# Performance work log

Hardware: AMD Instinct MI355X
Metric: run time of the kernel (lower is better)

Reference implementation:

```python
import jax, jax.numpy as jnp
import numpy as np

B, T, D = 4, 2048, 512
E, H, K = 8, 512, 2


def setup_inputs() -> dict:
    key = jax.random.key(0)
    ks = jax.random.split(key, 8)
    s_in = 1.0 / np.sqrt(D)
    s_h = 1.0 / np.sqrt(H)
    return {
        "x": jax.random.normal(ks[0], (B, T, D), dtype=jnp.float32),
        "Wg": jax.random.uniform(ks[1], (D, E), jnp.float32, -s_in, s_in),
        "bg": jax.random.uniform(ks[2], (E,), jnp.float32, -s_in, s_in),
        "W1": jax.random.uniform(ks[3], (E, D, H), jnp.float32, -s_in, s_in),
        "b1": jax.random.uniform(ks[4], (E, H), jnp.float32, -s_in, s_in),
        "W2": jax.random.uniform(ks[5], (E, H, H), jnp.float32, -s_h, s_h),
        "b2": jax.random.uniform(ks[6], (E, H), jnp.float32, -s_h, s_h),
    }


def reference(x, Wg, bg, W1, b1, W2, b2):
    Bx, Tx, Dx = x.shape
    xf = x.reshape(-1, Dx)                                   # [N, D]
    # --- gate (noise_std = 0) ---
    logits = xf @ Wg + bg                                    # [N, E]
    topk_scores, topk_idx = jax.lax.top_k(logits, K)         # [N, K]
    topk_w = jax.nn.softmax(topk_scores, axis=-1)            # K=2 -> softmax over selected
    # --- experts: dense compute, then gather the selected ones ---
    h = jax.nn.gelu(jnp.einsum('nd,edh->neh', xf, W1) + b1, approximate=False)  # [N, E, H]
    y = jnp.einsum('neh,ehf->nef', h, W2) + b2               # [N, E, H]
    sel = jnp.take_along_axis(y, topk_idx[:, :, None], axis=1)  # [N, K, H]
    out = jnp.sum(topk_w[:, :, None] * sel, axis=1)          # weighted combine [N, H]
    return out.reshape(Bx, Tx, -1)
```

## Files before the change

### kernel.cpp

```cpp
#include <hip/hip_runtime.h>
#include <hip/hip_bf16.h>


typedef __bf16 bf16x8 __attribute__((ext_vector_type(8)));
typedef float  f32x4  __attribute__((ext_vector_type(4)));

#define N_TOK 8192
#define D_IN  512
#define N_EXP 8
#define H_DIM 512
#define TILE  64

static __device__ __forceinline__ unsigned short f2bf(float f) {
    union { float f; unsigned u; } v; v.f = f;
    unsigned r = v.u + 0x7FFFu + ((v.u >> 16) & 1u);
    return (unsigned short)(r >> 16);
}
static __device__ __forceinline__ float bf2f(unsigned short h) {
    union { unsigned u; float f; } v; v.u = ((unsigned)h) << 16; return v.f;
}

__global__ void __launch_bounds__(256) k_pack(const float* __restrict__ W1,
                                              const float* __restrict__ W2,
                                              unsigned short* __restrict__ w1f,
                                              unsigned short* __restrict__ w2f) {
    __shared__ float t[32][65];
    int z = blockIdx.z;
    int e = z & 7;
    const float* in = (z < 8) ? W1 : W2;
    unsigned short* out = (z < 8) ? w1f : w2f;
    int cb0 = blockIdx.x * 4;
    int kc  = blockIdx.y;
    const float* src = in + ((size_t)e * 512 + kc * 32) * 512 + blockIdx.x * 64;
    int tid = threadIdx.x;
    int r = tid >> 3, cq = (tid & 7) * 8;
    float4 v0 = *(const float4*)(src + (size_t)r * 512 + cq);
    float4 v1 = *(const float4*)(src + (size_t)r * 512 + cq + 4);
    t[r][cq + 0] = v0.x; t[r][cq + 1] = v0.y; t[r][cq + 2] = v0.z; t[r][cq + 3] = v0.w;
    t[r][cq + 4] = v1.x; t[r][cq + 5] = v1.y; t[r][cq + 6] = v1.z; t[r][cq + 7] = v1.w;
    __syncthreads();
    int g = tid >> 6, lane = tid & 63;
    int l15 = lane & 15, l4 = lane >> 4;
    unsigned v[4];
    #pragma unroll
    for (int j = 0; j < 4; ++j) {
        unsigned lo = f2bf(t[l4 * 8 + 2 * j    ][g * 16 + l15]);
        unsigned hi = f2bf(t[l4 * 8 + 2 * j + 1][g * 16 + l15]);
        v[j] = lo | (hi << 16);
    }
    size_t dst = (((size_t)(e * 32 + cb0 + g) * 16 + kc) * 512) + lane * 8;
    *(uint4*)(out + dst) = make_uint4(v[0], v[1], v[2], v[3]);
}

__global__ void __launch_bounds__(256) k_gate(const float* __restrict__ x,
                                              const float* __restrict__ Wg,
                                              const float* __restrict__ bg,
                                              unsigned char* __restrict__ sel,
                                              float2* __restrict__ w2) {
    __shared__ float part[32][8][8];
    __shared__ float lg[32][8];
    int tid = threadIdx.x;
    int t = tid >> 3, c = tid & 7;
    int n = blockIdx.x * 32 + t;
    const float4* xr = (const float4*)(x + (size_t)n * D_IN + c * 64);
    float acc[8];
    #pragma unroll
    for (int e = 0; e < 8; ++e) acc[e] = 0.f;
    #pragma unroll
    for (int j4 = 0; j4 < 16; ++j4) {
        float4 v = xr[j4];
        int k = c * 64 + j4 * 4;
        float xv[4] = {v.x, v.y, v.z, v.w};
        #pragma unroll
        for (int u = 0; u < 4; ++u) {
            float4 wlo = *(const float4*)(Wg + (size_t)(k + u) * 8);
            float4 whi = *(const float4*)(Wg + (size_t)(k + u) * 8 + 4);
            acc[0] += xv[u] * wlo.x; acc[1] += xv[u] * wlo.y;
            acc[2] += xv[u] * wlo.z; acc[3] += xv[u] * wlo.w;
            acc[4] += xv[u] * whi.x; acc[5] += xv[u] * whi.y;
            acc[6] += xv[u] * whi.z; acc[7] += xv[u] * whi.w;
        }
    }
    #pragma unroll
    for (int e = 0; e < 8; ++e) part[t][c][e] = acc[e];
    __syncthreads();
    {
        float f = bg[c];
        #pragma unroll
        for (int cc = 0; cc < 8; ++cc) f += part[t][cc][c];
        lg[t][c] = f;
    }
    __syncthreads();
    if (c == 0) {
        float best = lg[t][0]; int i1 = 0;
        #pragma unroll
        for (int j = 1; j < 8; ++j) { float v = lg[t][j]; if (v > best) { best = v; i1 = j; } }
        float best2 = -1e30f; int i2 = 0;
        #pragma unroll
        for (int j = 0; j < 8; ++j) {
            if (j == i1) continue;
            float v = lg[t][j]; if (v > best2) { best2 = v; i2 = j; }
        }
        float tt = expf(best2 - best);
        float w0 = 1.0f / (1.0f + tt);
        sel[n] = (unsigned char)(i1 | (i2 << 4));
        w2[n] = make_float2(w0, 1.0f - w0);
    }
}

__global__ void __launch_bounds__(1024) k_build(const unsigned char* __restrict__ sel,
                                                const float2* __restrict__ w2,
                                                int* __restrict__ counts,
                                                int* __restrict__ lists,
                                                float* __restrict__ wgts) {
    int e = blockIdx.x;
    __shared__ int wave_tot[16], wave_base[16];
    int tid = threadIdx.x;
    int lane = tid & 63, wv = tid >> 6;
    int base = 0;
    for (int c0 = 0; c0 < N_TOK; c0 += 1024) {
        int n = c0 + tid;
        unsigned char s = sel[n];
        bool f1 = ((s & 15) == e);
        bool f = f1 || ((s >> 4) == e);
        unsigned long long mask = __ballot(f);
        int prefix = __popcll(mask & ((1ull << lane) - 1ull));
        if (lane == 0) wave_tot[wv] = __popcll(mask);
        __syncthreads();
        if (tid < 16) {
            int wb = 0;
            for (int i = 0; i < tid; ++i) wb += wave_tot[i];
            wave_base[tid] = wb;
        }
        __syncthreads();
        if (f) {
            int pos = base + wave_base[wv] + prefix;
            lists[e * N_TOK + pos] = (n << 1) | (f1 ? 0 : 1);
            float2 w = w2[n];
            wgts[e * N_TOK + pos] = f1 ? w.x : w.y;
        }
        base += wave_base[15] + wave_tot[15];
        __syncthreads();
    }
    if (tid == 0) counts[e] = base;
}

template <bool SLOT>
__global__ void __launch_bounds__(512, 2)
k_experts(const float* __restrict__ x,
          const unsigned short* __restrict__ w1f, const float* __restrict__ b1,
          const unsigned short* __restrict__ w2f, const float* __restrict__ b2,
          const int* __restrict__ counts, const int* __restrict__ lists,
          const float* __restrict__ wgts,
          unsigned short* __restrict__ ybuf, float* __restrict__ out) {
    __shared__ unsigned short ldsA[32 * D_IN];
    __shared__ unsigned short ldsB[32 * D_IN];
    __shared__ int   tl[TILE];
    __shared__ float wl[TILE];

    int b = blockIdx.x;
    int e = b & 7;
    int tile = b >> 3;
    int cnt = counts[e];
    int row0 = tile * TILE;
    if (row0 >= cnt) return;
    int rv = min(TILE, cnt - row0);

    int tid = threadIdx.x;
    int lane = tid & 63;
    int wid = tid >> 6;
    int cw = wid * 64;
    int l15 = lane & 15, l4 = lane >> 4;

    if (tid < TILE) {
        int v = 0; float w = 0.f;
        if (tid < rv) {
            v = lists[e * N_TOK + row0 + tid];
            w = wgts [e * N_TOK + row0 + tid];
        }
        tl[tid] = v; wl[tid] = w;
    }
    __syncthreads();

    #pragma unroll
    for (int it = 0; it < 16; ++it) {
        int idx = tid + it * 512;
        int r = idx >> 7, c4 = idx & 127;
        float4 v = make_float4(0.f, 0.f, 0.f, 0.f);
        if (r < rv)
            v = ((const float4*)(x + (size_t)(tl[r] >> 1) * D_IN))[c4];
        unsigned lo = (unsigned)f2bf(v.x) | ((unsigned)f2bf(v.y) << 16);
        unsigned hi = (unsigned)f2bf(v.z) | ((unsigned)f2bf(v.w) << 16);
        int rr = r & 31;
        int off = (rr * 1024 + c4 * 8) ^ ((rr & 7) << 4);
        char* base = (r < 32) ? (char*)ldsA : (char*)ldsB;
        *(uint2*)(base + off) = make_uint2(lo, hi);
    }
    __syncthreads();

    f32x4 accA[2][4], accB[2][4];

    {
        const unsigned short* wbase = w1f + ((size_t)(e * 32 + wid * 4) * 16) * 512 + (size_t)lane * 8;
        #pragma unroll
        for (int n = 0; n < 4; ++n) {
            float bv = b1[e * H_DIM + cw + n * 16 + l15];
            #pragma unroll
            for (int m = 0; m < 2; ++m) { accA[m][n] = f32x4{bv, bv, bv, bv}; accB[m][n] = f32x4{bv, bv, bv, bv}; }
        }
        bf16x8 bb[4][4];
        #pragma unroll
        for (int n = 0; n < 4; ++n) {
            bb[0][n] = *(const bf16x8*)(wbase + (n * 16 + 0) * 512);
            bb[1][n] = *(const bf16x8*)(wbase + (n * 16 + 1) * 512);
            bb[2][n] = *(const bf16x8*)(wbase + (n * 16 + 2) * 512);
        }
        #pragma unroll
        for (int kc = 0; kc < 16; ++kc) {
            if (kc + 3 < 16) {
                #pragma unroll
                for (int n = 0; n < 4; ++n)
                    bb[(kc + 3) & 3][n] = *(const bf16x8*)(wbase + (n * 16 + kc + 3) * 512);
            }
            int k0 = kc * 32 + l4 * 8;
            bf16x8 aA[2], aB[2];
            #pragma unroll
            for (int m = 0; m < 2; ++m) {
                int row = m * 16 + l15;
                int off = (row * 1024 + k0 * 2) ^ ((row & 7) << 4);
                aA[m] = *(const bf16x8*)((const char*)ldsA + off);
                aB[m] = *(const bf16x8*)((const char*)ldsB + off);
            }
            #pragma unroll
            for (int n = 0; n < 4; ++n) {
                #pragma unroll
                for (int m = 0; m < 2; ++m) {
                    accA[m][n] = __builtin_amdgcn_mfma_f32_16x16x32_bf16(aA[m], bb[kc & 3][n], accA[m][n], 0, 0, 0);
                    accB[m][n] = __builtin_amdgcn_mfma_f32_16x16x32_bf16(aB[m], bb[kc & 3][n], accB[m][n], 0, 0, 0);
                }
            }
        }
    }
    __syncthreads();

    #pragma unroll
    for (int m = 0; m < 2; ++m)
        #pragma unroll
        for (int n = 0; n < 4; ++n)
            #pragma unroll
            for (int r = 0; r < 4; ++r) {
                int row = m * 16 + l4 * 4 + r;
                int col = cw + n * 16 + l15;
                int off = (row * 1024 + col * 2) ^ ((row & 7) << 4);
                float vA = accA[m][n][r];
                float gA = 0.5f * vA * (1.0f + erff(vA * 0.70710678118654752f));
                *(unsigned short*)((char*)ldsA + off) = f2bf(gA);
                float vB = accB[m][n][r];
                float gB = 0.5f * vB * (1.0f + erff(vB * 0.70710678118654752f));
                *(unsigned short*)((char*)ldsB + off) = f2bf(gB);
            }
    __syncthreads();

    {
        const unsigned short* wbase = w2f + ((size_t)(e * 32 + wid * 4) * 16) * 512 + (size_t)lane * 8;
        #pragma unroll
        for (int n = 0; n < 4; ++n) {
            float bv = b2[e * H_DIM + cw + n * 16 + l15];
            #pragma unroll
            for (int m = 0; m < 2; ++m) { accA[m][n] = f32x4{bv, bv, bv, bv}; accB[m][n] = f32x4{bv, bv, bv, bv}; }
        }
        bf16x8 bb[4][4];
        #pragma unroll
        for (int n = 0; n < 4; ++n) {
            bb[0][n] = *(const bf16x8*)(wbase + (n * 16 + 0) * 512);
            bb[1][n] = *(const bf16x8*)(wbase + (n * 16 + 1) * 512);
            bb[2][n] = *(const bf16x8*)(wbase + (n * 16 + 2) * 512);
        }
        #pragma unroll
        for (int kc = 0; kc < 16; ++kc) {
            if (kc + 3 < 16) {
                #pragma unroll
                for (int n = 0; n < 4; ++n)
                    bb[(kc + 3) & 3][n] = *(const bf16x8*)(wbase + (n * 16 + kc + 3) * 512);
            }
            int k0 = kc * 32 + l4 * 8;
            bf16x8 aA[2], aB[2];
            #pragma unroll
            for (int m = 0; m < 2; ++m) {
                int row = m * 16 + l15;
                int off = (row * 1024 + k0 * 2) ^ ((row & 7) << 4);
                aA[m] = *(const bf16x8*)((const char*)ldsA + off);
                aB[m] = *(const bf16x8*)((const char*)ldsB + off);
            }
            #pragma unroll
            for (int n = 0; n < 4; ++n) {
                #pragma unroll
                for (int m = 0; m < 2; ++m) {
                    accA[m][n] = __builtin_amdgcn_mfma_f32_16x16x32_bf16(aA[m], bb[kc & 3][n], accA[m][n], 0, 0, 0);
                    accB[m][n] = __builtin_amdgcn_mfma_f32_16x16x32_bf16(aB[m], bb[kc & 3][n], accB[m][n], 0, 0, 0);
                }
            }
        }
    }

    if (SLOT) {
        __syncthreads();
        #pragma unroll
        for (int m = 0; m < 2; ++m)
            #pragma unroll
            for (int n = 0; n < 4; ++n)
                #pragma unroll
                for (int r = 0; r < 4; ++r) {
                    int row = m * 16 + l4 * 4 + r;
                    int col = cw + n * 16 + l15;
                    ldsA[row * 512 + col] = f2bf(accA[m][n][r] * wl[row]);
                    ldsB[row * 512 + col] = f2bf(accB[m][n][r] * wl[row + 32]);
                }
        __syncthreads();
        #pragma unroll
        for (int rr = 0; rr < 8; ++rr) {
            int row = wid * 8 + rr;
            if (row < rv) {
                int v = tl[row];
                const unsigned short* src = (row < 32) ? ldsA : ldsB;
                uint4 d = *(uint4*)((char*)src + (row & 31) * 1024 + lane * 16);
                *(uint4*)(ybuf + (size_t)v * H_DIM + lane * 8) = d;
            }
        }
    } else {
        #pragma unroll
        for (int m = 0; m < 2; ++m)
            #pragma unroll
            for (int r = 0; r < 4; ++r) {
                int rowA = m * 16 + l4 * 4 + r;
                int rowB = rowA + 32;
                #pragma unroll
                for (int n = 0; n < 4; ++n) {
                    int col = cw + n * 16 + l15;
                    if (rowA < rv)
                        atomicAdd(out + (size_t)(tl[rowA] >> 1) * H_DIM + col, wl[rowA] * accA[m][n][r]);
                    if (rowB < rv)
                        atomicAdd(out + (size_t)(tl[rowB] >> 1) * H_DIM + col, wl[rowB] * accB[m][n][r]);
                }
            }
    }
}

__global__ void __launch_bounds__(256) k_combine(const unsigned short* __restrict__ yb,
                                                 float* __restrict__ out) {
    int gid = blockIdx.x * 256 + threadIdx.x;
    int n = gid >> 6;
    int h0 = (gid & 63) * 8;
    const unsigned short* r0 = yb + ((size_t)2 * n) * H_DIM + h0;
    uint4 a = *(const uint4*)r0;
    uint4 b = *(const uint4*)(r0 + H_DIM);
    float o[8];
    unsigned ua[4] = {a.x, a.y, a.z, a.w}, ub[4] = {b.x, b.y, b.z, b.w};
    #pragma unroll
    for (int j = 0; j < 4; ++j) {
        o[2 * j]     = bf2f((unsigned short)(ua[j] & 0xFFFF)) + bf2f((unsigned short)(ub[j] & 0xFFFF));
        o[2 * j + 1] = bf2f((unsigned short)(ua[j] >> 16))    + bf2f((unsigned short)(ub[j] >> 16));
    }
    float* dst = out + (size_t)n * H_DIM + h0;
    *(float4*)dst       = make_float4(o[0], o[1], o[2], o[3]);
    *(float4*)(dst + 4) = make_float4(o[4], o[5], o[6], o[7]);
}

extern "C" void kernel_launch(void* const* d_in, const int* in_sizes, int n_in,
                              void* d_out, int out_size, void* d_ws, size_t ws_size,
                              hipStream_t stream) {
    (void)in_sizes; (void)n_in;
    const float* x  = (const float*)d_in[0];
    const float* Wg = (const float*)d_in[1];
    const float* bg = (const float*)d_in[2];
    const float* W1 = (const float*)d_in[3];
    const float* b1 = (const float*)d_in[4];
    const float* W2 = (const float*)d_in[5];
    const float* b2 = (const float*)d_in[6];
    float* out = (float*)d_out;

    char* ws = (char*)d_ws;
    unsigned short* w1f = (unsigned short*)(ws);
    unsigned short* w2f = (unsigned short*)(ws + (4u << 20));
    unsigned short* ybuf= (unsigned short*)(ws + (8u << 20));
    char* tail = ws + (24u << 20);
    int*   counts = (int*)(tail);
    int*   lists  = (int*)(tail + 256);
    float* wgts   = (float*)(tail + 256 + 262144);
    unsigned char* sel = (unsigned char*)(tail + 256 + 524288);
    float2* w2g   = (float2*)(tail + 256 + 532480);
    size_t need = (24u << 20) + 256 + 532480 + 65536;

    bool slot = ws_size >= need;
    if (!slot) {
        tail = ws + (8u << 20);
        counts = (int*)(tail);
        lists  = (int*)(tail + 256);
        wgts   = (float*)(tail + 256 + 262144);
        sel    = (unsigned char*)(tail + 256 + 524288);
        w2g    = (float2*)(tail + 256 + 532480);
        hipMemsetAsync(out, 0, (size_t)out_size * sizeof(float), stream);
    }

    k_pack<<<dim3(8, 16, 16), dim3(256), 0, stream>>>(W1, W2, w1f, w2f);
    k_gate<<<dim3(N_TOK / 32), dim3(256), 0, stream>>>(x, Wg, bg, sel, w2g);
    k_build<<<dim3(N_EXP), dim3(1024), 0, stream>>>(sel, w2g, counts, lists, wgts);
    if (slot) {
        k_experts<true><<<dim3(1024), dim3(512), 0, stream>>>(
            x, w1f, b1, w2f, b2, counts, lists, wgts, ybuf, out);
        k_combine<<<dim3(N_TOK * 64 / 256), dim3(256), 0, stream>>>(ybuf, out);
    } else {
        k_experts<false><<<dim3(1024), dim3(512), 0, stream>>>(
            x, w1f, b1, w2f, b2, counts, lists, wgts, ybuf, out);
    }
}
```

Baseline: 188.1 us.

## Merge pack and gate kernels; double expert block to 1024 threads

Weight packing and gating now run as one launch with branched block roles, removing one kernel launch and letting the two independent jobs overlap. The expert kernel uses 1024 threads (16 waves), each owning 32 output columns instead of 64. That halves per-wave accumulators and B-fragment registers, so more waves can hide latency. It also prefetches W1 fragments and biases before the token-gather barrier and W2 fragments before the epilogue barrier. The cost is lower per-wave reuse of the LDS A tiles: each A fragment feeds half as many MFMAs, and the 64 KB of LDS per block may cap occupancy.

```diff
diff --git a/kernel.cpp b/kernel.cpp
--- a/kernel.cpp
+++ b/kernel.cpp
@@ -20,91 +20,92 @@
     union { unsigned u; float f; } v; v.u = ((unsigned)h) << 16; return v.f;
 }
 
-__global__ void __launch_bounds__(256) k_pack(const float* __restrict__ W1,
+__global__ void __launch_bounds__(256) k_prep(const float* __restrict__ x,
+                                              const float* __restrict__ Wg,
+                                              const float* __restrict__ bg,
+                                              const float* __restrict__ W1,
                                               const float* __restrict__ W2,
                                               unsigned short* __restrict__ w1f,
-                                              unsigned short* __restrict__ w2f) {
-    __shared__ float t[32][65];
-    int z = blockIdx.z;
-    int e = z & 7;
-    const float* in = (z < 8) ? W1 : W2;
-    unsigned short* out = (z < 8) ? w1f : w2f;
-    int cb0 = blockIdx.x * 4;
-    int kc  = blockIdx.y;
-    const float* src = in + ((size_t)e * 512 + kc * 32) * 512 + blockIdx.x * 64;
-    int tid = threadIdx.x;
-    int r = tid >> 3, cq = (tid & 7) * 8;
-    float4 v0 = *(const float4*)(src + (size_t)r * 512 + cq);
-    float4 v1 = *(const float4*)(src + (size_t)r * 512 + cq + 4);
-    t[r][cq + 0] = v0.x; t[r][cq + 1] = v0.y; t[r][cq + 2] = v0.z; t[r][cq + 3] = v0.w;
-    t[r][cq + 4] = v1.x; t[r][cq + 5] = v1.y; t[r][cq + 6] = v1.z; t[r][cq + 7] = v1.w;
-    __syncthreads();
-    int g = tid >> 6, lane = tid & 63;
-    int l15 = lane & 15, l4 = lane >> 4;
-    unsigned v[4];
-    #pragma unroll
-    for (int j = 0; j < 4; ++j) {
-        unsigned lo = f2bf(t[l4 * 8 + 2 * j    ][g * 16 + l15]);
-        unsigned hi = f2bf(t[l4 * 8 + 2 * j + 1][g * 16 + l15]);
-        v[j] = lo | (hi << 16);
-    }
-    size_t dst = (((size_t)(e * 32 + cb0 + g) * 16 + kc) * 512) + lane * 8;
-    *(uint4*)(out + dst) = make_uint4(v[0], v[1], v[2], v[3]);
-}
-
-__global__ void __launch_bounds__(256) k_gate(const float* __restrict__ x,
-                                              const float* __restrict__ Wg,
-                                              const float* __restrict__ bg,
+                                              unsigned short* __restrict__ w2f,
                                               unsigned char* __restrict__ sel,
                                               float2* __restrict__ w2) {
+    __shared__ float t[32][65];
     __shared__ float part[32][8][8];
     __shared__ float lg[32][8];
+    int b = blockIdx.x;
     int tid = threadIdx.x;
-    int t = tid >> 3, c = tid & 7;
-    int n = blockIdx.x * 32 + t;
-    const float4* xr = (const float4*)(x + (size_t)n * D_IN + c * 64);
-    float acc[8];
-    #pragma unroll
-    for (int e = 0; e < 8; ++e) acc[e] = 0.f;
-    #pragma unroll
-    for (int j4 = 0; j4 < 16; ++j4) {
-        float4 v = xr[j4];
-        int k = c * 64 + j4 * 4;
-        float xv[4] = {v.x, v.y, v.z, v.w};
-        #pragma unroll
-        for (int u = 0; u < 4; ++u) {
-            float4 wlo = *(const float4*)(Wg + (size_t)(k + u) * 8);
-            float4 whi = *(const float4*)(Wg + (size_t)(k + u) * 8 + 4);
-            acc[0] += xv[u] * wlo.x; acc[1] += xv[u] * wlo.y;
-            acc[2] += xv[u] * wlo.z; acc[3] += xv[u] * wlo.w;
-            acc[4] += xv[u] * whi.x; acc[5] += xv[u] * whi.y;
-            acc[6] += xv[u] * whi.z; acc[7] += xv[u] * whi.w;
-        }
-    }
-    #pragma unroll
-    for (int e = 0; e < 8; ++e) part[t][c][e] = acc[e];
-    __syncthreads();
-    {
-        float f = bg[c];
-        #pragma unroll
-        for (int cc = 0; cc < 8; ++cc) f += part[t][cc][c];
-        lg[t][c] = f;
-    }
-    __syncthreads();
-    if (c == 0) {
-        float best = lg[t][0]; int i1 = 0;
-        #pragma unroll
-        for (int j = 1; j < 8; ++j) { float v = lg[t][j]; if (v > best) { best = v; i1 = j; } }
-        float best2 = -1e30f; int i2 = 0;
-        #pragma unroll
-        for (int j = 0; j < 8; ++j) {
-            if (j == i1) continue;
-            float v = lg[t][j]; if (v > best2) { best2 = v; i2 = j; }
-        }
-        float tt = expf(best2 - best);
-        float w0 = 1.0f / (1.0f + tt);
-        sel[n] = (unsigned char)(i1 | (i2 << 4));
-        w2[n] = make_float2(w0, 1.0f - w0);
+    if (b < 2048) {
+        int z = b >> 7, rem = b & 127;
+        int bx = rem & 7, kc = rem >> 3;
+        int e = z & 7;
+        const float* in = (z < 8) ? W1 : W2;
+        unsigned short* out = (z < 8) ? w1f : w2f;
+        const float* src = in + ((size_t)e * 512 + kc * 32) * 512 + bx * 64;
+        int r = tid >> 3, cq = (tid & 7) * 8;
+        float4 v0 = *(const float4*)(src + (size_t)r * 512 + cq);
+        float4 v1 = *(const float4*)(src + (size_t)r * 512 + cq + 4);
+        t[r][cq + 0] = v0.x; t[r][cq + 1] = v0.y; t[r][cq + 2] = v0.z; t[r][cq + 3] = v0.w;
+        t[r][cq + 4] = v1.x; t[r][cq + 5] = v1.y; t[r][cq + 6] = v1.z; t[r][cq + 7] = v1.w;
+        __syncthreads();
+        int g = tid >> 6, lane = tid & 63;
+        int l15 = lane & 15, l4 = lane >> 4;
+        unsigned v[4];
+        #pragma unroll
+        for (int j = 0; j < 4; ++j) {
+            unsigned lo = f2bf(t[l4 * 8 + 2 * j    ][g * 16 + l15]);
+            unsigned hi = f2bf(t[l4 * 8 + 2 * j + 1][g * 16 + l15]);
+            v[j] = lo | (hi << 16);
+        }
+        size_t dst = (((size_t)(e * 32 + bx * 4 + g) * 16 + kc) * 512) + lane * 8;
+        *(uint4*)(out + dst) = make_uint4(v[0], v[1], v[2], v[3]);
+    } else {
+        int gb = b - 2048;
+        int tt = tid >> 3, c = tid & 7;
+        int n = gb * 32 + tt;
+        const float4* xr = (const float4*)(x + (size_t)n * D_IN + c * 64);
+        float acc[8];
+        #pragma unroll
+        for (int e = 0; e < 8; ++e) acc[e] = 0.f;
+        #pragma unroll
+        for (int j4 = 0; j4 < 16; ++j4) {
+            float4 v = xr[j4];
+            int k = c * 64 + j4 * 4;
+            float xv[4] = {v.x, v.y, v.z, v.w};
+            #pragma unroll
+            for (int u = 0; u < 4; ++u) {
+                float4 wlo = *(const float4*)(Wg + (size_t)(k + u) * 8);
+                float4 whi = *(const float4*)(Wg + (size_t)(k + u) * 8 + 4);
+                acc[0] += xv[u] * wlo.x; acc[1] += xv[u] * wlo.y;
+                acc[2] += xv[u] * wlo.z; acc[3] += xv[u] * wlo.w;
+                acc[4] += xv[u] * whi.x; acc[5] += xv[u] * whi.y;
+                acc[6] += xv[u] * whi.z; acc[7] += xv[u] * whi.w;
+            }
+        }
+        #pragma unroll
+        for (int e = 0; e < 8; ++e) part[tt][c][e] = acc[e];
+        __syncthreads();
+        {
+            float f = bg[c];
+            #pragma unroll
+            for (int cc = 0; cc < 8; ++cc) f += part[tt][cc][c];
+            lg[tt][c] = f;
+        }
+        __syncthreads();
+        if (c == 0) {
+            float best = lg[tt][0]; int i1 = 0;
+            #pragma unroll
+            for (int j = 1; j < 8; ++j) { float v = lg[tt][j]; if (v > best) { best = v; i1 = j; } }
+            float best2 = -1e30f; int i2 = 0;
+            #pragma unroll
+            for (int j = 0; j < 8; ++j) {
+                if (j == i1) continue;
+                float v = lg[tt][j]; if (v > best2) { best2 = v; i2 = j; }
+            }
+            float e2 = expf(best2 - best);
+            float w0 = 1.0f / (1.0f + e2);
+            sel[n] = (unsigned char)(i1 | (i2 << 4));
+            w2[n] = make_float2(w0, 1.0f - w0);
+        }
     }
 }
 
@@ -146,7 +147,7 @@
 }
 
 template <bool SLOT>
-__global__ void __launch_bounds__(512, 2)
+__global__ void __launch_bounds__(1024, 4)
 k_experts(const float* __restrict__ x,
           const unsigned short* __restrict__ w1f, const float* __restrict__ b1,
           const unsigned short* __restrict__ w2f, const float* __restrict__ b2,
@@ -169,7 +170,7 @@
     int tid = threadIdx.x;
     int lane = tid & 63;
     int wid = tid >> 6;
-    int cw = wid * 64;
+    int cw = wid * 32;
     int l15 = lane & 15, l4 = lane >> 4;
 
     if (tid < TILE) {
@@ -180,11 +181,27 @@
         }
         tl[tid] = v; wl[tid] = w;
     }
+
+    const unsigned short* w1base = w1f + ((size_t)(e * 32 + wid * 2) * 16) * 512 + (size_t)lane * 8;
+    const unsigned short* w2base = w2f + ((size_t)(e * 32 + wid * 2) * 16) * 512 + (size_t)lane * 8;
+    bf16x8 bb[4][2];
+    #pragma unroll
+    for (int n = 0; n < 2; ++n) {
+        bb[0][n] = *(const bf16x8*)(w1base + (n * 16 + 0) * 512);
+        bb[1][n] = *(const bf16x8*)(w1base + (n * 16 + 1) * 512);
+        bb[2][n] = *(const bf16x8*)(w1base + (n * 16 + 2) * 512);
+    }
+    float bv1[2], bv2[2];
+    #pragma unroll
+    for (int n = 0; n < 2; ++n) {
+        bv1[n] = b1[e * H_DIM + cw + n * 16 + l15];
+        bv2[n] = b2[e * H_DIM + cw + n * 16 + l15];
+    }
     __syncthreads();
 
     #pragma unroll
-    for (int it = 0; it < 16; ++it) {
-        int idx = tid + it * 512;
+    for (int it = 0; it < 8; ++it) {
+        int idx = tid + it * 1024;
         int r = idx >> 7, c4 = idx & 127;
         float4 v = make_float4(0.f, 0.f, 0.f, 0.f);
         if (r < rv)
@@ -198,55 +215,52 @@
     }
     __syncthreads();
 
-    f32x4 accA[2][4], accB[2][4];
-
-    {
-        const unsigned short* wbase = w1f + ((size_t)(e * 32 + wid * 4) * 16) * 512 + (size_t)lane * 8;
-        #pragma unroll
-        for (int n = 0; n < 4; ++n) {
-            float bv = b1[e * H_DIM + cw + n * 16 + l15];
-            #pragma unroll
-            for (int m = 0; m < 2; ++m) { accA[m][n] = f32x4{bv, bv, bv, bv}; accB[m][n] = f32x4{bv, bv, bv, bv}; }
-        }
-        bf16x8 bb[4][4];
-        #pragma unroll
-        for (int n = 0; n < 4; ++n) {
-            bb[0][n] = *(const bf16x8*)(wbase + (n * 16 + 0) * 512);
-            bb[1][n] = *(const bf16x8*)(wbase + (n * 16 + 1) * 512);
-            bb[2][n] = *(const bf16x8*)(wbase + (n * 16 + 2) * 512);
-        }
-        #pragma unroll
-        for (int kc = 0; kc < 16; ++kc) {
-            if (kc + 3 < 16) {
-                #pragma unroll
-                for (int n = 0; n < 4; ++n)
-                    bb[(kc + 3) & 3][n] = *(const bf16x8*)(wbase + (n * 16 + kc + 3) * 512);
-            }
-            int k0 = kc * 32 + l4 * 8;
-            bf16x8 aA[2], aB[2];
+    f32x4 accA[2][2], accB[2][2];
+
+    #pragma unroll
+    for (int n = 0; n < 2; ++n)
+        #pragma unroll
+        for (int m = 0; m < 2; ++m) {
+            accA[m][n] = f32x4{bv1[n], bv1[n], bv1[n], bv1[n]};
+            accB[m][n] = f32x4{bv1[n], bv1[n], bv1[n], bv1[n]};
+        }
+    #pragma unroll
+    for (int kc = 0; kc < 16; ++kc) {
+        if (kc + 3 < 16) {
+            #pragma unroll
+            for (int n = 0; n < 2; ++n)
+                bb[(kc + 3) & 3][n] = *(const bf16x8*)(w1base + (n * 16 + kc + 3) * 512);
+        }
+        int k0 = kc * 32 + l4 * 8;
+        bf16x8 aA[2], aB[2];
+        #pragma unroll
+        for (int m = 0; m < 2; ++m) {
+            int row = m * 16 + l15;
+            int off = (row * 1024 + k0 * 2) ^ ((row & 7) << 4);
+            aA[m] = *(const bf16x8*)((const char*)ldsA + off);
+            aB[m] = *(const bf16x8*)((const char*)ldsB + off);
+        }
+        #pragma unroll
+        for (int n = 0; n < 2; ++n)
             #pragma unroll
             for (int m = 0; m < 2; ++m) {
-                int row = m * 16 + l15;
-                int off = (row * 1024 + k0 * 2) ^ ((row & 7) << 4);
-                aA[m] = *(const bf16x8*)((const char*)ldsA + off);
-                aB[m] = *(const bf16x8*)((const char*)ldsB + off);
-            }
-            #pragma unroll
-            for (int n = 0; n < 4; ++n) {
-                #pragma unroll
-                for (int m = 0; m < 2; ++m) {
-                    accA[m][n] = __builtin_amdgcn_mfma_f32_16x16x32_bf16(aA[m], bb[kc & 3][n], accA[m][n], 0, 0, 0);
-                    accB[m][n] = __builtin_amdgcn_mfma_f32_16x16x32_bf16(aB[m], bb[kc & 3][n], accB[m][n], 0, 0, 0);
-                }
-            }
-        }
+                accA[m][n] = __builtin_amdgcn_mfma_f32_16x16x32_bf16(aA[m], bb[kc & 3][n], accA[m][n], 0, 0, 0);
+                accB[m][n] = __builtin_amdgcn_mfma_f32_16x16x32_bf16(aB[m], bb[kc & 3][n], accB[m][n], 0, 0, 0);
+            }
+    }
+
+    #pragma unroll
+    for (int n = 0; n < 2; ++n) {
+        bb[0][n] = *(const bf16x8*)(w2base + (n * 16 + 0) * 512);
+        bb[1][n] = *(const bf16x8*)(w2base + (n * 16 + 1) * 512);
+        bb[2][n] = *(const bf16x8*)(w2base + (n * 16 + 2) * 512);
     }
     __syncthreads();
 
     #pragma unroll
     for (int m = 0; m < 2; ++m)
         #pragma unroll
-        for (int n = 0; n < 4; ++n)
+        for (int n = 0; n < 2; ++n)
             #pragma unroll
             for (int r = 0; r < 4; ++r) {
                 int row = m * 16 + l4 * 4 + r;
@@ -261,46 +275,36 @@
             }
     __syncthreads();
 
-    {
-        const unsigned short* wbase = w2f + ((size_t)(e * 32 + wid * 4) * 16) * 512 + (size_t)lane * 8;
-        #pragma unroll
-        for (int n = 0; n < 4; ++n) {
-            float bv = b2[e * H_DIM + cw + n * 16 + l15];
-            #pragma unroll
-            for (int m = 0; m < 2; ++m) { accA[m][n] = f32x4{bv, bv, bv, bv}; accB[m][n] = f32x4{bv, bv, bv, bv}; }
-        }
-        bf16x8 bb[4][4];
-        #pragma unroll
-        for (int n = 0; n < 4; ++n) {
-            bb[0][n] = *(const bf16x8*)(wbase + (n * 16 + 0) * 512);
-            bb[1][n] = *(const bf16x8*)(wbase + (n * 16 + 1) * 512);
-            bb[2][n] = *(const bf16x8*)(wbase + (n * 16 + 2) * 512);
-        }
-        #pragma unroll
-        for (int kc = 0; kc < 16; ++kc) {
-            if (kc + 3 < 16) {
-                #pragma unroll
-                for (int n = 0; n < 4; ++n)
-                    bb[(kc + 3) & 3][n] = *(const bf16x8*)(wbase + (n * 16 + kc + 3) * 512);
-            }
-            int k0 = kc * 32 + l4 * 8;
-            bf16x8 aA[2], aB[2];
+    #pragma unroll
+    for (int n = 0; n < 2; ++n)
+        #pragma unroll
+        for (int m = 0; m < 2; ++m) {
+            accA[m][n] = f32x4{bv2[n], bv2[n], bv2[n], bv2[n]};
+            accB[m][n] = f32x4{bv2[n], bv2[n], bv2[n], bv2[n]};
+        }
+    #pragma unroll
+    for (int kc = 0; kc < 16; ++kc) {
+        if (kc + 3 < 16) {
+            #pragma unroll
+            for (int n = 0; n < 2; ++n)
+                bb[(kc + 3) & 3][n] = *(const bf16x8*)(w2base + (n * 16 + kc + 3) * 512);
+        }
+        int k0 = kc * 32 + l4 * 8;
+        bf16x8 aA[2], aB[2];
+        #pragma unroll
+        for (int m = 0; m < 2; ++m) {
+            int row = m * 16 + l15;
+            int off = (row * 1024 + k0 * 2) ^ ((row & 7) << 4);
+            aA[m] = *(const bf16x8*)((const char*)ldsA + off);
+            aB[m] = *(const bf16x8*)((const char*)ldsB + off);
+        }
+        #pragma unroll
+        for (int n = 0; n < 2; ++n)
             #pragma unroll
             for (int m = 0; m < 2; ++m) {
-                int row = m * 16 + l15;
-                int off = (row * 1024 + k0 * 2) ^ ((row & 7) << 4);
-                aA[m] = *(const bf16x8*)((const char*)ldsA + off);
-                aB[m] = *(const bf16x8*)((const char*)ldsB + off);
-            }
-            #pragma unroll
-            for (int n = 0; n < 4; ++n) {
-                #pragma unroll
-                for (int m = 0; m < 2; ++m) {
-                    accA[m][n] = __builtin_amdgcn_mfma_f32_16x16x32_bf16(aA[m], bb[kc & 3][n], accA[m][n], 0, 0, 0);
-                    accB[m][n] = __builtin_amdgcn_mfma_f32_16x16x32_bf16(aB[m], bb[kc & 3][n], accB[m][n], 0, 0, 0);
-                }
-            }
-        }
+                accA[m][n] = __builtin_amdgcn_mfma_f32_16x16x32_bf16(aA[m], bb[kc & 3][n], accA[m][n], 0, 0, 0);
+                accB[m][n] = __builtin_amdgcn_mfma_f32_16x16x32_bf16(aB[m], bb[kc & 3][n], accB[m][n], 0, 0, 0);
+            }
     }
 
     if (SLOT) {
@@ -308,7 +312,7 @@
         #pragma unroll
         for (int m = 0; m < 2; ++m)
             #pragma unroll
-            for (int n = 0; n < 4; ++n)
+            for (int n = 0; n < 2; ++n)
                 #pragma unroll
                 for (int r = 0; r < 4; ++r) {
                     int row = m * 16 + l4 * 4 + r;
@@ -318,8 +322,8 @@
                 }
         __syncthreads();
         #pragma unroll
-        for (int rr = 0; rr < 8; ++rr) {
-            int row = wid * 8 + rr;
+        for (int rr = 0; rr < 4; ++rr) {
+            int row = wid * 4 + rr;
             if (row < rv) {
                 int v = tl[row];
                 const unsigned short* src = (row < 32) ? ldsA : ldsB;
@@ -335,7 +339,7 @@
                 int rowA = m * 16 + l4 * 4 + r;
                 int rowB = rowA + 32;
                 #pragma unroll
-                for (int n = 0; n < 4; ++n) {
+                for (int n = 0; n < 2; ++n) {
                     int col = cw + n * 16 + l15;
                     if (rowA < rv)
                         atomicAdd(out + (size_t)(tl[rowA] >> 1) * H_DIM + col, wl[rowA] * accA[m][n][r]);
@@ -402,15 +406,15 @@
         hipMemsetAsync(out, 0, (size_t)out_size * sizeof(float), stream);
     }
 
-    k_pack<<<dim3(8, 16, 16), dim3(256), 0, stream>>>(W1, W2, w1f, w2f);
-    k_gate<<<dim3(N_TOK / 32), dim3(256), 0, stream>>>(x, Wg, bg, sel, w2g);
+    k_prep<<<dim3(2048 + N_TOK / 32), dim3(256), 0, stream>>>(
+        x, Wg, bg, W1, W2, w1f, w2f, sel, w2g);
     k_build<<<dim3(N_EXP), dim3(1024), 0, stream>>>(sel, w2g, counts, lists, wgts);
     if (slot) {
-        k_experts<true><<<dim3(1024), dim3(512), 0, stream>>>(
+        k_experts<true><<<dim3(1024), dim3(1024), 0, stream>>>(
             x, w1f, b1, w2f, b2, counts, lists, wgts, ybuf, out);
         k_combine<<<dim3(N_TOK * 64 / 256), dim3(256), 0, stream>>>(ybuf, out);
     } else {
-        k_experts<false><<<dim3(1024), dim3(512), 0, stream>>>(
+        k_experts<false><<<dim3(1024), dim3(1024), 0, stream>>>(
             x, w1f, b1, w2f, b2, counts, lists, wgts, ybuf, out);
     }
 }
```

Result: slower. 208.3 us (+10.7%).
